# Kernel tuning notes

Measured on AMD Instinct MI355X. Metric: run time of the kernel, lower is better.

Reference implementation:

```python
import jax, jax.numpy as jnp
import numpy as np

B = 512; S = 2048; K = 128; E = 64; A = 128; H = 4; DK = A // H; OD = 64; BITS = 32
FOH = 15; FMH = 4; FSP = 4; LSP = 50
VOH = 10001; VMH = 100001; VSP = 10001
D0 = 27 * E


def _short_attn(tgt, seq, mask, qW, qb, kW, kb, vW, vb, oW, ob):
    # tgt [F,b,1,E], seq [F,b,s,E], mask [F,b,1,s] bool
    F_, b_, s_, _ = seq.shape
    q = (jnp.einsum('fbte,fea->fbta', tgt, qW) + qb[:, None, None, :]).reshape(F_, b_, -1, H, DK)
    k = (jnp.einsum('fbse,fea->fbsa', seq, kW) + kb[:, None, None, :]).reshape(F_, b_, s_, H, DK)
    v = (jnp.einsum('fbse,fea->fbsa', seq, vW) + vb[:, None, None, :]).reshape(F_, b_, s_, H, DK)
    scores = jnp.einsum('fbthd,fbshd->fbhts', q, k) / (DK ** 0.5)
    scores = jnp.where(mask[:, :, None, :, :], scores, -jnp.inf)
    attn = jax.nn.softmax(scores, axis=-1)
    out = jnp.einsum('fbhts,fbshd->fbthd', attn, v).reshape(F_, b_, -1, A)
    return jnp.einsum('fbta,fao->fbto', out, oW) + ob[:, None, None, :]  # [F,b,1,OD]


def _forward(one_hot_tables, multi_hot_tables, special_tables, hash_weights,
             sqW, sqb, skW, skb, svW, svb, soW, sob,
             lqW, lqb, lkW, lkb, lvW, lvb, loW, lob,
             W0, b0, W1, b1, W2, b2, outW, outb,
             one_hot_ids, multi_hot_ids, special_ids):
    lookup = jax.vmap(lambda t, i: t[i], in_axes=(0, 0))
    oh_emb = jax.vmap(lambda t, i: t[i], in_axes=(0, 1))(one_hot_tables, one_hot_ids)  # [FOH,B,E]
    mh_mask = multi_hot_ids >= 0                                                       # [FMH,B,S]
    mh_emb = lookup(multi_hot_tables, jnp.where(mh_mask, multi_hot_ids, 0))            # [FMH,B,S,E]
    sp_mask = special_ids >= 0
    sp_emb = (lookup(special_tables, jnp.where(sp_mask, special_ids, 0))
              * sp_mask[..., None].astype(jnp.float32)).sum(axis=2)                    # [FSP,B,E] sum combiner
    tgt = oh_emb[:FMH][:, :, None, :]  # targets = first 4 one-hot fields, [4,B,1,E]
    # short attention over first K candidates of each history
    short = _short_attn(tgt, mh_emb[:, :, :K, :], mh_mask[:, :, None, :K],
                        sqW, sqb, skW, skb, svW, svb, soW, sob)                        # [4,B,1,OD]
    # long attention: LSH hash -> hamming-sim topk -> gather -> attention
    th = (jnp.einsum('fbe,eh->fbh', tgt[:, :, 0, :], hash_weights) > 0).astype(jnp.float32)
    sh = (jnp.einsum('fbse,eh->fbsh', mh_emb, hash_weights) > 0).astype(jnp.float32)
    sim = -jnp.sum(jnp.abs(sh - th[:, :, None, :]), axis=-1)                           # [4,B,S]
    sim = jnp.where(mh_mask, sim, -jnp.inf)
    _, idx = jax.lax.top_k(sim, K)                                                     # [4,B,K]
    topk_seq = jnp.take_along_axis(mh_emb, idx[..., None], axis=2)                     # [4,B,K,E]
    topk_mask = jnp.take_along_axis(mh_mask, idx, axis=2)[:, :, None, :]
    long = _short_attn(tgt, topk_seq, topk_mask,
                       lqW, lqb, lkW, lkb, lvW, lvb, loW, lob)                         # [4,B,1,OD]
    b_ = oh_emb.shape[1]
    feats = jnp.concatenate([
        oh_emb.transpose(1, 0, 2).reshape(b_, -1),
        sp_emb.transpose(1, 0, 2).reshape(b_, -1),
        short[:, :, 0, :].transpose(1, 0, 2).reshape(b_, -1),
        long[:, :, 0, :].transpose(1, 0, 2).reshape(b_, -1)], axis=-1)                 # [B, 27*E]
    x = jax.nn.relu(feats @ W0 + b0)
    x = jax.nn.relu(x @ W1 + b1)
    x = jax.nn.relu(x @ W2 + b2)
    logits = (x @ outW + outb)[:, 0]
    return jax.nn.sigmoid(logits), logits


def setup_inputs():
    ks = list(jax.random.split(jax.random.key(0), 64))
    def nrm(shape, scale):
        return jax.random.normal(ks.pop(), shape, dtype=jnp.float32) * scale
    std = (2.0 / 512.0) ** 0.5
    d = {}
    d['one_hot_tables'] = nrm((FOH, VOH, E), std)
    d['multi_hot_tables'] = nrm((FMH, VMH, E), std)
    d['special_tables'] = nrm((FSP, VSP, E), std)
    d['hash_weights'] = nrm((E, BITS), 1.0)
    for p in ('s', 'l'):
        d[p + 'qW'] = nrm((FMH, E, A), E ** -0.5); d[p + 'qb'] = nrm((FMH, A), 0.01)
        d[p + 'kW'] = nrm((FMH, E, A), E ** -0.5); d[p + 'kb'] = nrm((FMH, A), 0.01)
        d[p + 'vW'] = nrm((FMH, E, A), E ** -0.5); d[p + 'vb'] = nrm((FMH, A), 0.01)
        d[p + 'oW'] = nrm((FMH, A, OD), A ** -0.5); d[p + 'ob'] = nrm((FMH, OD), 0.01)
    dims = [D0, 1024, 512, 256]
    for i in range(3):
        d['W%d' % i] = nrm((dims[i], dims[i + 1]), dims[i] ** -0.5)
        d['b%d' % i] = nrm((dims[i + 1],), 0.01)
    d['outW'] = nrm((256, 1), 256 ** -0.5)
    d['outb'] = nrm((1,), 0.01)
    d['one_hot_ids'] = jax.random.randint(ks.pop(), (B, FOH), 0, VOH, dtype=jnp.int32)
    d['multi_hot_ids'] = jax.random.randint(ks.pop(), (FMH, B, S), 0, VMH, dtype=jnp.int32)
    d['special_ids'] = jax.random.randint(ks.pop(), (FSP, B, LSP), 0, VSP, dtype=jnp.int32)
    return d


def reference(one_hot_tables, multi_hot_tables, special_tables, hash_weights, sqW, sqb, skW, skb, svW, svb, soW, sob, lqW, lqb, lkW, lkb, lvW, lvb, loW, lob, W0, b0, W1, b1, W2, b2, outW, outb, one_hot_ids, multi_hot_ids, special_ids):
    return _forward(one_hot_tables, multi_hot_tables, special_tables, hash_weights,
                    sqW, sqb, skW, skb, svW, svb, soW, sob,
                    lqW, lqb, lkW, lkb, lvW, lvb, loW, lob,
                    W0, b0, W1, b1, W2, b2, outW, outb,
                    one_hot_ids, multi_hot_ids, special_ids)
```

## Files before the change

### kernel.cpp

```cpp
#include <hip/hip_runtime.h>
#include <math.h>

#define F_MH 4
#define NB   512
#define SEQ  2048
#define TOPK 128
#define EDIM 64
#define ADIM 128
#define VOH  10001
#define VMH  100001
#define NROWS (F_MH * VMH)
#define D0   1728
#define RSQRT32 0.17677669529663687f

typedef __bf16 bf16x8 __attribute__((ext_vector_type(8)));
typedef __bf16 bf16x4 __attribute__((ext_vector_type(4)));
typedef float  f32x4  __attribute__((ext_vector_type(4)));

__global__ __launch_bounds__(128) void k_hash(const float* __restrict__ tab,
                                              const float* __restrict__ hw,
                                              unsigned int* __restrict__ sig)
{
    __shared__ float rows[128][65];
    const int t = threadIdx.x;
    const float4* __restrict__ hw4 = (const float4*)hw;
    const long long base_dw = (long long)blockIdx.x * 32768;
    const long long lim = (long long)NROWS * 64;
    float4 pf[16];
#pragma unroll
    for (int i = 0; i < 16; ++i) {
        const long long idx = base_dw + i * 512 + t * 4;
        pf[i] = make_float4(0.f, 0.f, 0.f, 0.f);
        if (idx < lim) pf[i] = *(const float4*)(tab + idx);
    }
    for (int c = 0; c < 4; ++c) {
        __syncthreads();
#pragma unroll
        for (int i = 0; i < 16; ++i) {
            const int idx = i * 512 + t * 4;
            const int row = idx >> 6, e = idx & 63;
            rows[row][e + 0] = pf[i].x; rows[row][e + 1] = pf[i].y;
            rows[row][e + 2] = pf[i].z; rows[row][e + 3] = pf[i].w;
        }
        __syncthreads();
        if (c < 3) {
#pragma unroll
            for (int i = 0; i < 16; ++i) {
                const long long idx = base_dw + (long long)(c + 1) * 8192 + i * 512 + t * 4;
                pf[i] = make_float4(0.f, 0.f, 0.f, 0.f);
                if (idx < lim) pf[i] = *(const float4*)(tab + idx);
            }
        }
        float4 acc[8];
#pragma unroll
        for (int h = 0; h < 8; ++h) acc[h] = make_float4(0.f, 0.f, 0.f, 0.f);
#pragma unroll 16
        for (int e = 0; e < 64; ++e) {
            const float x = rows[t][e];
#pragma unroll
            for (int h = 0; h < 8; ++h) {
                const float4 w = hw4[e * 8 + h];
                acc[h].x += x * w.x; acc[h].y += x * w.y;
                acc[h].z += x * w.z; acc[h].w += x * w.w;
            }
        }
        unsigned int bits = 0u;
#pragma unroll
        for (int h = 0; h < 8; ++h) {
            bits |= (acc[h].x > 0.f ? 1u : 0u) << (h * 4);
            bits |= (acc[h].y > 0.f ? 2u : 0u) << (h * 4);
            bits |= (acc[h].z > 0.f ? 4u : 0u) << (h * 4);
            bits |= (acc[h].w > 0.f ? 8u : 0u) << (h * 4);
        }
        const int r = blockIdx.x * 512 + c * 128 + t;
        if (r < NROWS) sig[r] = bits;
    }
}

__global__ __launch_bounds__(256) void k_topk(const float* __restrict__ oh_tab,
                                              const float* __restrict__ hw,
                                              const unsigned int* __restrict__ sig,
                                              const int* __restrict__ oh_ids,
                                              const int* __restrict__ mh_ids,
                                              int* __restrict__ sel)
{
    const int b = blockIdx.x, f = blockIdx.y, t = threadIdx.x;
    __shared__ float tgt[64];
    __shared__ unsigned int thbits;
    __shared__ int hist[34];
    __shared__ int c_lt[256], c_eq[256];
    __shared__ int s_dstar, s_cntlt;
    if (t < 64) tgt[t] = oh_tab[((size_t)f * VOH + oh_ids[b * 15 + f]) * 64 + t];
    if (t == 0) thbits = 0u;
    if (t < 34) hist[t] = 0;
    __syncthreads();
    if (t < 32) {
        float acc = 0.f;
#pragma unroll
        for (int e = 0; e < 64; ++e) acc += tgt[e] * hw[e * 32 + t];
        if (acc > 0.f) atomicOr(&thbits, 1u << t);
    }
    __syncthreads();
    const unsigned int th = thbits;
    const int* idp = mh_ids + (size_t)(f * NB + b) * SEQ + t * 8;
    int ids[8], dv[8];
#pragma unroll
    for (int j = 0; j < 8; ++j) {
        int id = idp[j];
        ids[j] = id;
        int d = (id >= 0) ? __popc(sig[f * VMH + id] ^ th) : 33;
        dv[j] = d;
        atomicAdd(&hist[d], 1);
    }
    __syncthreads();
    if (t == 0) {
        int cum = 0, ds = 33, cl = 0;
        for (int d = 0; d <= 33; ++d) {
            if (cum + hist[d] >= TOPK) { ds = d; cl = cum; break; }
            cum += hist[d];
        }
        s_dstar = ds; s_cntlt = cl;
    }
    __syncthreads();
    const int Dstar = s_dstar, cntlt = s_cntlt;
    int nlt = 0, neq = 0;
#pragma unroll
    for (int j = 0; j < 8; ++j) {
        nlt += (dv[j] < Dstar);
        neq += (dv[j] == Dstar);
    }
    c_lt[t] = nlt; c_eq[t] = neq;
    __syncthreads();
    for (int off = 1; off < 256; off <<= 1) {
        int vl = 0, ve = 0;
        if (t >= off) { vl = c_lt[t - off]; ve = c_eq[t - off]; }
        __syncthreads();
        c_lt[t] += vl; c_eq[t] += ve;
        __syncthreads();
    }
    int lt_pos = c_lt[t] - nlt;
    int eq_pos = cntlt + c_eq[t] - neq;
    int* selp = sel + (size_t)(f * NB + b) * TOPK;
#pragma unroll
    for (int j = 0; j < 8; ++j) {
        if (dv[j] < Dstar) { selp[lt_pos++] = ids[j]; }
        else if (dv[j] == Dstar) {
            if (eq_pos < TOPK) selp[eq_pos] = ids[j];
            eq_pos++;
        }
    }
}

__global__ __launch_bounds__(256) void k_attn(const float* __restrict__ oh_tab,
                                              const float* __restrict__ mh_tab,
                                              const int* __restrict__ oh_ids,
                                              const int* __restrict__ mh_ids,
                                              const int* __restrict__ sel,
                                              const float* __restrict__ sqW, const float* __restrict__ sqb,
                                              const float* __restrict__ skW, const float* __restrict__ skb,
                                              const float* __restrict__ svW, const float* __restrict__ svb,
                                              const float* __restrict__ soW, const float* __restrict__ sob,
                                              const float* __restrict__ lqW, const float* __restrict__ lqb,
                                              const float* __restrict__ lkW, const float* __restrict__ lkb,
                                              const float* __restrict__ lvW, const float* __restrict__ lvb,
                                              const float* __restrict__ loW, const float* __restrict__ lob,
                                              __bf16* __restrict__ feats)
{
    const int b = blockIdx.x, f = blockIdx.y, z = blockIdx.z, t = threadIdx.x;
    const float* WQ = (z ? lqW : sqW) + (size_t)f * (EDIM * ADIM);
    const float* bq = (z ? lqb : sqb) + f * ADIM;
    const float* WK = (z ? lkW : skW) + (size_t)f * (EDIM * ADIM);
    const float* bk = (z ? lkb : skb) + f * ADIM;
    const float* WV = (z ? lvW : svW) + (size_t)f * (EDIM * ADIM);
    const float* bv = (z ? lvb : svb) + f * ADIM;
    const float* WO = (z ? loW : soW) + (size_t)f * (ADIM * 64);
    const float* bo = (z ? lob : sob) + f * 64;

    __shared__ float tgt[64];
    __shared__ int   sid[128];
    __shared__ float seqT[64][132];
    __shared__ float qv[128];
    __shared__ float qk[4][64];
    __shared__ float qkb4[4];
    __shared__ float sc[4][128];
    __shared__ float wemb[4][64];
    __shared__ float outv[128];

    if (t < 64) tgt[t] = oh_tab[((size_t)f * VOH + oh_ids[b * 15 + f]) * 64 + t];
    if (t < 128) {
        int id;
        if (z == 0) id = mh_ids[(size_t)(f * NB + b) * SEQ + t];
        else        id = sel[(size_t)(f * NB + b) * TOPK + t];
        sid[t] = id;
    }
    __syncthreads();
#pragma unroll
    for (int i = 0; i < 8; ++i) {
        int v = t + i * 256;
        int row = v >> 4, c4 = (v & 15) << 2;
        int id = sid[row];
        float4 ev = make_float4(0.f, 0.f, 0.f, 0.f);
        if (id >= 0) ev = *(const float4*)&mh_tab[((size_t)f * VMH + id) * 64 + c4];
        seqT[c4 + 0][row] = ev.x; seqT[c4 + 1][row] = ev.y;
        seqT[c4 + 2][row] = ev.z; seqT[c4 + 3][row] = ev.w;
    }
    if (t < 128) {
        float acc = bq[t];
#pragma unroll
        for (int e = 0; e < 64; ++e) acc += tgt[e] * WQ[e * 128 + t];
        qv[t] = acc;
    }
    __syncthreads();
    {
        const int h = t >> 6, e = t & 63;
        float acc = 0.f;
#pragma unroll
        for (int d = 0; d < 32; ++d) acc += qv[h * 32 + d] * WK[e * 128 + h * 32 + d];
        qk[h][e] = acc * RSQRT32;
    }
    if (t < 4) {
        float acc = 0.f;
#pragma unroll
        for (int d = 0; d < 32; ++d) acc += qv[t * 32 + d] * bk[t * 32 + d];
        qkb4[t] = acc * RSQRT32;
    }
    __syncthreads();
#pragma unroll
    for (int rep = 0; rep < 2; ++rep) {
        int idx = t + rep * 256;
        int h = idx >> 7, s = idx & 127;
        float acc = qkb4[h];
#pragma unroll
        for (int e4 = 0; e4 < 16; ++e4) {
            float4 q4 = *(const float4*)&qk[h][e4 * 4];
            acc += seqT[e4 * 4 + 0][s] * q4.x + seqT[e4 * 4 + 1][s] * q4.y
                 + seqT[e4 * 4 + 2][s] * q4.z + seqT[e4 * 4 + 3][s] * q4.w;
        }
        sc[h][s] = (sid[s] >= 0) ? acc : -INFINITY;
    }
    __syncthreads();
    {
        const int h = t >> 6, l = t & 63;
        float v0 = sc[h][l], v1 = sc[h][l + 64];
        float m = fmaxf(v0, v1);
        for (int off = 32; off; off >>= 1) m = fmaxf(m, __shfl_xor(m, off));
        float p0 = expf(v0 - m), p1 = expf(v1 - m);
        float ssum = p0 + p1;
        for (int off = 32; off; off >>= 1) ssum += __shfl_xor(ssum, off);
        float inv = 1.f / ssum;
        sc[h][l] = p0 * inv; sc[h][l + 64] = p1 * inv;
    }
    __syncthreads();
    {
        const int h = t >> 6, e = t & 63;
        float acc = 0.f;
#pragma unroll
        for (int s4 = 0; s4 < 32; ++s4) {
            float4 a4 = *(const float4*)&sc[h][s4 * 4];
            float4 e4 = *(const float4*)&seqT[e][s4 * 4];
            acc += a4.x * e4.x + a4.y * e4.y + a4.z * e4.z + a4.w * e4.w;
        }
        wemb[h][e] = acc;
    }
    __syncthreads();
    if (t < 128) {
        const int h = t >> 5;
        float acc = bv[t];
#pragma unroll
        for (int e = 0; e < 64; ++e) acc += wemb[h][e] * WV[e * 128 + t];
        outv[t] = acc;
    }
    __syncthreads();
    if (t < 64) {
        float acc = bo[t];
#pragma unroll
        for (int a = 0; a < 128; ++a) acc += outv[a] * WO[a * 64 + t];
        feats[(size_t)b * D0 + (z ? 1472 : 1216) + f * 64 + t] = (__bf16)acc;
    }
}

__global__ __launch_bounds__(256) void k_feats(const float* __restrict__ oh_tab,
                                               const float* __restrict__ sp_tab,
                                               const int* __restrict__ oh_ids,
                                               const int* __restrict__ sp_ids,
                                               __bf16* __restrict__ feats)
{
    const int b = blockIdx.x, t = threadIdx.x;
    __shared__ int sidl[200];
    __shared__ int ohid[15];
    if (t < 200) sidl[t] = sp_ids[(size_t)((t / 50) * NB + b) * 50 + (t % 50)];
    if (t >= 240 && t < 255) ohid[t - 240] = oh_ids[b * 15 + (t - 240)];
    __syncthreads();
    __bf16* fr = feats + (size_t)b * D0;
    for (int p = t; p < 960; p += 256) {
        int f = p >> 6, e = p & 63;
        fr[p] = (__bf16)oh_tab[((size_t)f * VOH + ohid[f]) * 64 + e];
    }
    {
        int f = t >> 6, e = t & 63;
        float acc = 0.f;
        for (int j = 0; j < 50; ++j) {
            int id = sidl[f * 50 + j];
            if (id >= 0) acc += sp_tab[((size_t)f * VOH + id) * 64 + e];
        }
        fr[960 + t] = (__bf16)acc;
    }
}

__global__ __launch_bounds__(256) void k_trans(const float* __restrict__ W,
                                               __bf16* __restrict__ WT,
                                               int K, int N)
{
    __shared__ float tile[32][33];
    const int t = threadIdx.x;
    const int n0 = blockIdx.x * 32, k0 = blockIdx.y * 32;
    const int c = t & 31, r = t >> 5;
#pragma unroll
    for (int i = 0; i < 4; ++i)
        tile[r + 8 * i][c] = W[(size_t)(k0 + r + 8 * i) * N + n0 + c];
    __syncthreads();
#pragma unroll
    for (int i = 0; i < 4; ++i)
        WT[(size_t)(n0 + r + 8 * i) * K + k0 + c] = (__bf16)tile[c][r + 8 * i];
}

__global__ __launch_bounds__(256) void gemm_mfma(const __bf16* __restrict__ A,
                                                 const __bf16* __restrict__ BT,
                                                 const float* __restrict__ bias,
                                                 __bf16* __restrict__ C,
                                                 int M, int N, int K, int relu)
{
    __shared__ __bf16 As[64][72];
    __shared__ __bf16 Bs[64][72];
    const int t = threadIdx.x;
    const int n0 = blockIdx.x * 64, m0 = blockIdx.y * 64;
    const int wave = t >> 6, lane = t & 63;
    const int wm = (wave >> 1) * 32, wn = (wave & 1) * 32;
    const int row16 = lane & 15, quad = lane >> 4;
    f32x4 acc[2][2] = {};
    const int sr = t >> 3;
    const int sseg = (t & 7) * 8;
    for (int k0 = 0; k0 < K; k0 += 64) {
        bf16x8 av0 = *(const bf16x8*)&A[(size_t)(m0 + sr) * K + k0 + sseg];
        bf16x8 av1 = *(const bf16x8*)&A[(size_t)(m0 + sr + 32) * K + k0 + sseg];
        bf16x8 bv0 = *(const bf16x8*)&BT[(size_t)(n0 + sr) * K + k0 + sseg];
        bf16x8 bv1 = *(const bf16x8*)&BT[(size_t)(n0 + sr + 32) * K + k0 + sseg];
        __syncthreads();
        *(bf16x8*)&As[sr][sseg] = av0;
        *(bf16x8*)&As[sr + 32][sseg] = av1;
        *(bf16x8*)&Bs[sr][sseg] = bv0;
        *(bf16x8*)&Bs[sr + 32][sseg] = bv1;
        __syncthreads();
#pragma unroll
        for (int kk = 0; kk < 2; ++kk) {
            bf16x8 a0 = *(const bf16x8*)&As[wm + row16][kk * 32 + quad * 8];
            bf16x8 a1 = *(const bf16x8*)&As[wm + 16 + row16][kk * 32 + quad * 8];
            bf16x8 b0 = *(const bf16x8*)&Bs[wn + row16][kk * 32 + quad * 8];
            bf16x8 b1 = *(const bf16x8*)&Bs[wn + 16 + row16][kk * 32 + quad * 8];
            acc[0][0] = __builtin_amdgcn_mfma_f32_16x16x32_bf16(a0, b0, acc[0][0], 0, 0, 0);
            acc[0][1] = __builtin_amdgcn_mfma_f32_16x16x32_bf16(a0, b1, acc[0][1], 0, 0, 0);
            acc[1][0] = __builtin_amdgcn_mfma_f32_16x16x32_bf16(a1, b0, acc[1][0], 0, 0, 0);
            acc[1][1] = __builtin_amdgcn_mfma_f32_16x16x32_bf16(a1, b1, acc[1][1], 0, 0, 0);
        }
    }
#pragma unroll
    for (int i = 0; i < 2; ++i)
#pragma unroll
        for (int j = 0; j < 2; ++j) {
            const int col = n0 + wn + j * 16 + row16;
            const float bz = bias[col];
#pragma unroll
            for (int r = 0; r < 4; ++r) {
                const int rowm = m0 + wm + i * 16 + quad * 4 + r;
                float v = acc[i][j][r] + bz;
                if (relu) v = fmaxf(v, 0.f);
                C[(size_t)rowm * N + col] = (__bf16)v;
            }
        }
}

__global__ __launch_bounds__(256) void k_out(const __bf16* __restrict__ x2,
                                             const float* __restrict__ outW,
                                             const float* __restrict__ outb,
                                             float* __restrict__ out)
{
    const int t = threadIdx.x;
    const int wave = t >> 6, lane = t & 63;
    const int row = blockIdx.x * 4 + wave;
    bf16x4 xv = *(const bf16x4*)&x2[(size_t)row * 256 + lane * 4];
    const float4 wv = *(const float4*)&outW[lane * 4];
    float v = (float)xv[0] * wv.x + (float)xv[1] * wv.y
            + (float)xv[2] * wv.z + (float)xv[3] * wv.w;
    for (int off = 32; off; off >>= 1) v += __shfl_down(v, off);
    if (lane == 0) {
        float lg = v + outb[0];
        out[row] = 1.f / (1.f + expf(-lg));
        out[NB + row] = lg;
    }
}

extern "C" void kernel_launch(void* const* d_in, const int* in_sizes, int n_in,
                              void* d_out, int out_size, void* d_ws, size_t ws_size,
                              hipStream_t stream)
{
    const float* oh_tab = (const float*)d_in[0];
    const float* mh_tab = (const float*)d_in[1];
    const float* sp_tab = (const float*)d_in[2];
    const float* hw     = (const float*)d_in[3];
    const float* sqW = (const float*)d_in[4];  const float* sqb = (const float*)d_in[5];
    const float* skW = (const float*)d_in[6];  const float* skb = (const float*)d_in[7];
    const float* svW = (const float*)d_in[8];  const float* svb = (const float*)d_in[9];
    const float* soW = (const float*)d_in[10]; const float* sob = (const float*)d_in[11];
    const float* lqW = (const float*)d_in[12]; const float* lqb = (const float*)d_in[13];
    const float* lkW = (const float*)d_in[14]; const float* lkb = (const float*)d_in[15];
    const float* lvW = (const float*)d_in[16]; const float* lvb = (const float*)d_in[17];
    const float* loW = (const float*)d_in[18]; const float* lob = (const float*)d_in[19];
    const float* W0 = (const float*)d_in[20];  const float* b0 = (const float*)d_in[21];
    const float* W1 = (const float*)d_in[22];  const float* b1 = (const float*)d_in[23];
    const float* W2 = (const float*)d_in[24];  const float* b2 = (const float*)d_in[25];
    const float* outW = (const float*)d_in[26]; const float* outb = (const float*)d_in[27];
    const int* oh_ids = (const int*)d_in[28];
    const int* mh_ids = (const int*)d_in[29];
    const int* sp_ids = (const int*)d_in[30];

    char* ws = (char*)d_ws;
    unsigned int* sig = (unsigned int*)(ws + 0);
    int*    sel   = (int*)   (ws + 1600512);
    __bf16* feats = (__bf16*)(ws + 2649088);
    __bf16* x0    = (__bf16*)(ws + 4418560);
    __bf16* x1    = (__bf16*)(ws + 5467136);
    __bf16* x2    = (__bf16*)(ws + 5991424);
    __bf16* WT0   = (__bf16*)(ws + 6253568);
    __bf16* WT1   = (__bf16*)(ws + 9792512);
    __bf16* WT2   = (__bf16*)(ws + 10841088);

    k_trans<<<dim3(1024 / 32, 1728 / 32), 256, 0, stream>>>(W0, WT0, 1728, 1024);
    k_trans<<<dim3(512 / 32, 1024 / 32), 256, 0, stream>>>(W1, WT1, 1024, 512);
    k_trans<<<dim3(256 / 32, 512 / 32), 256, 0, stream>>>(W2, WT2, 512, 256);

    k_hash<<<(NROWS + 511) / 512, 128, 0, stream>>>(mh_tab, hw, sig);
    k_topk<<<dim3(NB, F_MH), 256, 0, stream>>>(oh_tab, hw, sig, oh_ids, mh_ids, sel);
    k_feats<<<NB, 256, 0, stream>>>(oh_tab, sp_tab, oh_ids, sp_ids, feats);
    k_attn<<<dim3(NB, F_MH, 2), 256, 0, stream>>>(oh_tab, mh_tab, oh_ids, mh_ids, sel,
                                                  sqW, sqb, skW, skb, svW, svb, soW, sob,
                                                  lqW, lqb, lkW, lkb, lvW, lvb, loW, lob,
                                                  feats);
    gemm_mfma<<<dim3(16, 8), 256, 0, stream>>>(feats, WT0, b0, x0, 512, 1024, 1728, 1);
    gemm_mfma<<<dim3(8, 8), 256, 0, stream>>>(x0, WT1, b1, x1, 512, 512, 1024, 1);
    gemm_mfma<<<dim3(4, 8), 256, 0, stream>>>(x1, WT2, b2, x2, 512, 256, 512, 1);
    k_out<<<NB / 4, 256, 0, stream>>>(x2, outW, outb, (float*)d_out);
}
```

Before: 466.6 us.

## Fold attention Q·K and V·O weights per head; stage hash weights in LDS

Adds a k_fold kernel that precomputes per-head products WQ·WKᵀ and WV·WO, plus folded biases. The attention kernel then computes query-key scores directly in embedding space and applies a single combined value-output projection, which removes several projection GEMVs and syncs per block. The sequence tile layout changes from transposed to row-major. The hash kernel now stages its hash weights in shared memory instead of reading them from global memory, and its unroll factor is reduced. The key bias is dropped because it is constant across positions and cancels in the softmax; the code also contains dead placeholder loops.

After: 484.6 us. 1.04x slower.

```diff
diff --git a/kernel.cpp b/kernel.cpp
--- a/kernel.cpp
+++ b/kernel.cpp
@@ -22,8 +22,10 @@
                                               unsigned int* __restrict__ sig)
 {
     __shared__ float rows[128][65];
+    __shared__ float4 hwl[512];
     const int t = threadIdx.x;
-    const float4* __restrict__ hw4 = (const float4*)hw;
+#pragma unroll
+    for (int i = 0; i < 4; ++i) hwl[t + i * 128] = ((const float4*)hw)[t + i * 128];
     const long long base_dw = (long long)blockIdx.x * 32768;
     const long long lim = (long long)NROWS * 64;
     float4 pf[16];
@@ -54,12 +56,12 @@
         float4 acc[8];
 #pragma unroll
         for (int h = 0; h < 8; ++h) acc[h] = make_float4(0.f, 0.f, 0.f, 0.f);
-#pragma unroll 16
+#pragma unroll 8
         for (int e = 0; e < 64; ++e) {
             const float x = rows[t][e];
 #pragma unroll
             for (int h = 0; h < 8; ++h) {
-                const float4 w = hw4[e * 8 + h];
+                const float4 w = hwl[e * 8 + h];
                 acc[h].x += x * w.x; acc[h].y += x * w.y;
                 acc[h].z += x * w.z; acc[h].w += x * w.w;
             }
@@ -151,40 +153,90 @@
     }
 }
 
-__global__ __launch_bounds__(256) void k_attn(const float* __restrict__ oh_tab,
-                                              const float* __restrict__ mh_tab,
-                                              const int* __restrict__ oh_ids,
-                                              const int* __restrict__ mh_ids,
-                                              const int* __restrict__ sel,
-                                              const float* __restrict__ sqW, const float* __restrict__ sqb,
-                                              const float* __restrict__ skW, const float* __restrict__ skb,
+__global__ __launch_bounds__(256) void k_fold(const float* __restrict__ sqW, const float* __restrict__ sqb,
+                                              const float* __restrict__ skW,
                                               const float* __restrict__ svW, const float* __restrict__ svb,
                                               const float* __restrict__ soW, const float* __restrict__ sob,
                                               const float* __restrict__ lqW, const float* __restrict__ lqb,
-                                              const float* __restrict__ lkW, const float* __restrict__ lkb,
+                                              const float* __restrict__ lkW,
                                               const float* __restrict__ lvW, const float* __restrict__ lvb,
                                               const float* __restrict__ loW, const float* __restrict__ lob,
-                                              __bf16* __restrict__ feats)
+                                              float* __restrict__ Mq, float* __restrict__ B1,
+                                              float* __restrict__ VO, float* __restrict__ bvo)
+{
+    const int f = blockIdx.x, z = blockIdx.y, h = blockIdx.z, t = threadIdx.x;
+    const float* WQ = (z ? lqW : sqW) + (size_t)f * 8192;
+    const float* bq = (z ? lqb : sqb) + f * 128;
+    const float* WK = (z ? lkW : skW) + (size_t)f * 8192;
+    const float* WV = (z ? lvW : svW) + (size_t)f * 8192;
+    const float* bv = (z ? lvb : svb) + f * 128;
+    const float* WO = (z ? loW : soW) + (size_t)f * 8192;
+    const float* bo = (z ? lob : sob) + f * 64;
+
+    __shared__ float wq[64][33], wk[64][33], wv[64][33], wo[32][65];
+#pragma unroll
+    for (int i = 0; i < 8; ++i) {
+        int j = t + i * 256;
+        wq[j >> 5][j & 31] = WQ[(j >> 5) * 128 + h * 32 + (j & 31)];
+        wk[j >> 5][j & 31] = WK[(j >> 5) * 128 + h * 32 + (j & 31)];
+        wv[j >> 5][j & 31] = WV[(j >> 5) * 128 + h * 32 + (j & 31)];
+        wo[j >> 6][j & 63] = WO[(h * 32 + (j >> 6)) * 64 + (j & 63)];
+    }
+    __syncthreads();
+    const int lane = t & 63, grp = t >> 6;
+    float* Mqb = Mq + (size_t)(((z * 4 + f) * 4 + h)) * 4096;
+    float* VOb = VO + (size_t)(((z * 4 + f) * 4 + h)) * 4096;
+#pragma unroll 4
+    for (int g = 0; g < 16; ++g) {
+        const int ep = grp * 16 + g;
+        float am = 0.f, av = 0.f;
+#pragma unroll
+        for (int d = 0; d < 32; ++d) {
+            am += wq[ep][d] * wk[lane][d];
+            av += wv[ep][d] * wo[d][lane];
+        }
+        Mqb[ep * 64 + lane] = am;
+        VOb[ep * 64 + lane] = av;
+    }
+    if (t < 64) {
+        float acc = 0.f;
+#pragma unroll
+        for (int d = 0; d < 32; ++d) acc += bq[h * 32 + d] * wk[t][d];
+        B1[((z * 4 + f) * 4 + h) * 64 + t] = acc;
+    }
+    if (h == 0 && t >= 64 && t < 128) {
+        const int o = t - 64;
+        float acc = bo[o];
+        for (int a = 0; a < 128; ++a) acc += bv[a] * WO[a * 64 + o];
+        bvo[(z * 4 + f) * 64 + o] = acc;
+    }
+}
+
+__global__ __launch_bounds__(256, 4) void k_attn(const float* __restrict__ oh_tab,
+                                                 const float* __restrict__ mh_tab,
+                                                 const int* __restrict__ oh_ids,
+                                                 const int* __restrict__ mh_ids,
+                                                 const int* __restrict__ sel,
+                                                 const float* __restrict__ Mq,
+                                                 const float* __restrict__ B1,
+                                                 const float* __restrict__ VO,
+                                                 const float* __restrict__ bvo,
+                                                 __bf16* __restrict__ feats)
 {
     const int b = blockIdx.x, f = blockIdx.y, z = blockIdx.z, t = threadIdx.x;
-    const float* WQ = (z ? lqW : sqW) + (size_t)f * (EDIM * ADIM);
-    const float* bq = (z ? lqb : sqb) + f * ADIM;
-    const float* WK = (z ? lkW : skW) + (size_t)f * (EDIM * ADIM);
-    const float* bk = (z ? lkb : skb) + f * ADIM;
-    const float* WV = (z ? lvW : svW) + (size_t)f * (EDIM * ADIM);
-    const float* bv = (z ? lvb : svb) + f * ADIM;
-    const float* WO = (z ? loW : soW) + (size_t)f * (ADIM * 64);
-    const float* bo = (z ? lob : sob) + f * 64;
-
+    const int zf = z * 4 + f;
+    const float* Mqb = Mq + (size_t)zf * 4 * 4096;
+    const float* B1b = B1 + zf * 4 * 64;
+    const float* VOb = VO + (size_t)zf * 4 * 4096;
+    const float* bvob = bvo + zf * 64;
+
+    __shared__ float seq[128][65];
     __shared__ float tgt[64];
     __shared__ int   sid[128];
-    __shared__ float seqT[64][132];
-    __shared__ float qv[128];
     __shared__ float qk[4][64];
-    __shared__ float qkb4[4];
     __shared__ float sc[4][128];
     __shared__ float wemb[4][64];
-    __shared__ float outv[128];
+    __shared__ float partial[4][64];
 
     if (t < 64) tgt[t] = oh_tab[((size_t)f * VOH + oh_ids[b * 15 + f]) * 64 + t];
     if (t < 128) {
@@ -194,47 +246,54 @@
         sid[t] = id;
     }
     __syncthreads();
+    float4 ev[2];
+#pragma unroll
+    for (int i = 0; i < 2; ++i) {
+        const int v = t + i * 256;
+        const int row = v >> 1, c4 = (v & 1) << 5;
+        (void)row; (void)c4;
+    }
+#pragma unroll
+    for (int i = 0; i < 2; ++i) {
+        const int v = t + i * 256;
+        const int row = v >> 2, c4 = (v & 3) << 4;
+        (void)row; (void)c4;
+    }
+    float4 g[8];
 #pragma unroll
     for (int i = 0; i < 8; ++i) {
-        int v = t + i * 256;
-        int row = v >> 4, c4 = (v & 15) << 2;
-        int id = sid[row];
-        float4 ev = make_float4(0.f, 0.f, 0.f, 0.f);
-        if (id >= 0) ev = *(const float4*)&mh_tab[((size_t)f * VMH + id) * 64 + c4];
-        seqT[c4 + 0][row] = ev.x; seqT[c4 + 1][row] = ev.y;
-        seqT[c4 + 2][row] = ev.z; seqT[c4 + 3][row] = ev.w;
-    }
-    if (t < 128) {
-        float acc = bq[t];
-#pragma unroll
-        for (int e = 0; e < 64; ++e) acc += tgt[e] * WQ[e * 128 + t];
-        qv[t] = acc;
-    }
-    __syncthreads();
+        const int v = t + i * 256;
+        const int row = v >> 4, c4 = (v & 15) << 2;
+        const int id = sid[row];
+        g[i] = make_float4(0.f, 0.f, 0.f, 0.f);
+        if (id >= 0) g[i] = *(const float4*)&mh_tab[((size_t)f * VMH + id) * 64 + c4];
+    }
     {
         const int h = t >> 6, e = t & 63;
+        float acc = B1b[h * 64 + e];
+        const float* mrow = Mqb + h * 4096 + e;
+#pragma unroll 16
+        for (int ep = 0; ep < 64; ++ep) acc += tgt[ep] * mrow[ep * 64];
+        qk[h][e] = acc * RSQRT32;
+    }
+#pragma unroll
+    for (int i = 0; i < 8; ++i) {
+        const int v = t + i * 256;
+        const int row = v >> 4, c4 = (v & 15) << 2;
+        seq[row][c4 + 0] = g[i].x; seq[row][c4 + 1] = g[i].y;
+        seq[row][c4 + 2] = g[i].z; seq[row][c4 + 3] = g[i].w;
+    }
+    __syncthreads();
+#pragma unroll
+    for (int rep = 0; rep < 2; ++rep) {
+        const int idx = t + rep * 256;
+        const int h = idx >> 7, s = idx & 127;
         float acc = 0.f;
 #pragma unroll
-        for (int d = 0; d < 32; ++d) acc += qv[h * 32 + d] * WK[e * 128 + h * 32 + d];
-        qk[h][e] = acc * RSQRT32;
-    }
-    if (t < 4) {
-        float acc = 0.f;
-#pragma unroll
-        for (int d = 0; d < 32; ++d) acc += qv[t * 32 + d] * bk[t * 32 + d];
-        qkb4[t] = acc * RSQRT32;
-    }
-    __syncthreads();
-#pragma unroll
-    for (int rep = 0; rep < 2; ++rep) {
-        int idx = t + rep * 256;
-        int h = idx >> 7, s = idx & 127;
-        float acc = qkb4[h];
-#pragma unroll
         for (int e4 = 0; e4 < 16; ++e4) {
-            float4 q4 = *(const float4*)&qk[h][e4 * 4];
-            acc += seqT[e4 * 4 + 0][s] * q4.x + seqT[e4 * 4 + 1][s] * q4.y
-                 + seqT[e4 * 4 + 2][s] * q4.z + seqT[e4 * 4 + 3][s] * q4.w;
+            const float4 q4 = *(const float4*)&qk[h][e4 * 4];
+            acc += seq[s][e4 * 4 + 0] * q4.x + seq[s][e4 * 4 + 1] * q4.y
+                 + seq[s][e4 * 4 + 2] * q4.z + seq[s][e4 * 4 + 3] * q4.w;
         }
         sc[h][s] = (sid[s] >= 0) ? acc : -INFINITY;
     }
@@ -250,31 +309,28 @@
         float inv = 1.f / ssum;
         sc[h][l] = p0 * inv; sc[h][l + 64] = p1 * inv;
     }
-    __syncthreads();
     {
         const int h = t >> 6, e = t & 63;
         float acc = 0.f;
-#pragma unroll
+#pragma unroll 8
         for (int s4 = 0; s4 < 32; ++s4) {
-            float4 a4 = *(const float4*)&sc[h][s4 * 4];
-            float4 e4 = *(const float4*)&seqT[e][s4 * 4];
-            acc += a4.x * e4.x + a4.y * e4.y + a4.z * e4.z + a4.w * e4.w;
+            const float4 a4 = *(const float4*)&sc[h][s4 * 4];
+            acc += a4.x * seq[s4 * 4 + 0][e] + a4.y * seq[s4 * 4 + 1][e]
+                 + a4.z * seq[s4 * 4 + 2][e] + a4.w * seq[s4 * 4 + 3][e];
         }
         wemb[h][e] = acc;
     }
-    __syncthreads();
-    if (t < 128) {
-        const int h = t >> 5;
-        float acc = bv[t];
-#pragma unroll
-        for (int e = 0; e < 64; ++e) acc += wemb[h][e] * WV[e * 128 + t];
-        outv[t] = acc;
+    {
+        const int h = t >> 6, o = t & 63;
+        float acc = 0.f;
+        const float* vrow = VOb + h * 4096 + o;
+#pragma unroll 16
+        for (int e = 0; e < 64; ++e) acc += wemb[h][e] * vrow[e * 64];
+        partial[h][o] = acc;
     }
     __syncthreads();
     if (t < 64) {
-        float acc = bo[t];
-#pragma unroll
-        for (int a = 0; a < 128; ++a) acc += outv[a] * WO[a * 64 + t];
+        float acc = partial[0][t] + partial[1][t] + partial[2][t] + partial[3][t] + bvob[t];
         feats[(size_t)b * D0 + (z ? 1472 : 1216) + f * 64 + t] = (__bf16)acc;
     }
 }
@@ -422,6 +478,7 @@
     const int* oh_ids = (const int*)d_in[28];
     const int* mh_ids = (const int*)d_in[29];
     const int* sp_ids = (const int*)d_in[30];
+    (void)skb; (void)lkb;
 
     char* ws = (char*)d_ws;
     unsigned int* sig = (unsigned int*)(ws + 0);
@@ -433,18 +490,23 @@
     __bf16* WT0   = (__bf16*)(ws + 6253568);
     __bf16* WT1   = (__bf16*)(ws + 9792512);
     __bf16* WT2   = (__bf16*)(ws + 10841088);
+    float*  Mq    = (float*) (ws + 11103232);
+    float*  VO    = (float*) (ws + 11627520);
+    float*  B1    = (float*) (ws + 12151808);
+    float*  bvo   = (float*) (ws + 12160000);
 
     k_trans<<<dim3(1024 / 32, 1728 / 32), 256, 0, stream>>>(W0, WT0, 1728, 1024);
     k_trans<<<dim3(512 / 32, 1024 / 32), 256, 0, stream>>>(W1, WT1, 1024, 512);
     k_trans<<<dim3(256 / 32, 512 / 32), 256, 0, stream>>>(W2, WT2, 512, 256);
+    k_fold<<<dim3(F_MH, 2, 4), 256, 0, stream>>>(sqW, sqb, skW, svW, svb, soW, sob,
+                                                 lqW, lqb, lkW, lvW, lvb, loW, lob,
+                                                 Mq, B1, VO, bvo);
 
     k_hash<<<(NROWS + 511) / 512, 128, 0, stream>>>(mh_tab, hw, sig);
     k_topk<<<dim3(NB, F_MH), 256, 0, stream>>>(oh_tab, hw, sig, oh_ids, mh_ids, sel);
     k_feats<<<NB, 256, 0, stream>>>(oh_tab, sp_tab, oh_ids, sp_ids, feats);
     k_attn<<<dim3(NB, F_MH, 2), 256, 0, stream>>>(oh_tab, mh_tab, oh_ids, mh_ids, sel,
-                                                  sqW, sqb, skW, skb, svW, svb, soW, sob,
-                                                  lqW, lqb, lkW, lkb, lvW, lvb, loW, lob,
-                                                  feats);
+                                                  Mq, B1, VO, bvo, feats);
     gemm_mfma<<<dim3(16, 8), 256, 0, stream>>>(feats, WT0, b0, x0, 512, 1024, 1728, 1);
     gemm_mfma<<<dim3(8, 8), 256, 0, stream>>>(x0, WT1, b1, x1, 512, 512, 1024, 1);
     gemm_mfma<<<dim3(4, 8), 256, 0, stream>>>(x1, WT2, b2, x2, 512, 256, 512, 1);
```
